# Kernel tuning notes

Measured on AMD Instinct MI355X. Metric: run time of the kernel, lower is better.

The kernel has to match this reference:

```python
import jax, jax.numpy as jnp
import numpy as np

B, H, V, L, NSTYLES = 16, 512, 32000, 3, 5


def setup_inputs() -> dict:
    key = jax.random.key(0)
    ks = jax.random.split(key, 9)
    s = 0.05  # weight init scale
    return {
        "context_vector": jax.random.normal(ks[0], (B, H), dtype=jnp.float32),
        "style_id": jax.random.randint(ks[1], (B,), 0, NSTYLES),
        "style_table": jax.random.normal(ks[2], (NSTYLES, H), dtype=jnp.float32) * s,
        "W_ih": jax.random.normal(ks[3], (L, 4 * H, H), dtype=jnp.float32) * s,
        "W_hh": jax.random.normal(ks[4], (L, 4 * H, H), dtype=jnp.float32) * s,
        "b_ih": jax.random.normal(ks[5], (L, 4 * H), dtype=jnp.float32) * s,
        "b_hh": jax.random.normal(ks[6], (L, 4 * H), dtype=jnp.float32) * s,
        "W_out": jax.random.normal(ks[7], (V, H), dtype=jnp.float32) * s,
        "b_out": jax.random.normal(ks[8], (V,), dtype=jnp.float32) * s,
        "max_length": 100,
    }


def _decode(context_vector, style_id, style_table, W_ih, W_hh, b_ih, b_hh, W_out, b_out, max_length):
    n_layers = W_ih.shape[0]
    x0 = style_table[style_id]                                   # [B, H] style embedding = first input token
    h0 = jnp.broadcast_to(context_vector[None], (n_layers,) + context_vector.shape)  # [L, B, H]
    c0 = jnp.zeros_like(h0)

    def step(carry, _):
        h, c, x = carry
        hs, cs, inp = [], [], x
        for l in range(n_layers):  # small fixed layer loop
            gates = inp @ W_ih[l].T + b_ih[l] + h[l] @ W_hh[l].T + b_hh[l]  # [B, 4H]
            i_g, f_g, g_g, o_g = jnp.split(gates, 4, axis=-1)  # PyTorch i,f,g,o order
            cn = jax.nn.sigmoid(f_g) * c[l] + jax.nn.sigmoid(i_g) * jnp.tanh(g_g)
            hn = jax.nn.sigmoid(o_g) * jnp.tanh(cn)
            hs.append(hn); cs.append(cn); inp = hn
        logits = inp @ W_out.T + b_out                            # [B, V]
        return (jnp.stack(hs), jnp.stack(cs), inp), logits

    _, logits_seq = jax.lax.scan(step, (h0, c0, x0), None, length=max_length)  # [T, B, V]
    # torch stacks [B,1,V] slices along dim=1 -> [B, T, 1, V]
    return jnp.transpose(logits_seq, (1, 0, 2))[:, :, None, :]


def reference(context_vector, style_id, style_table, W_ih, W_hh, b_ih, b_hh, W_out, b_out, max_length):
    return _decode(context_vector, style_id, style_table, W_ih, W_hh, b_ih, b_hh, W_out, b_out, max_length)
```

## Files before the change

### kernel.cpp

```cpp
#include <hip/hip_runtime.h>
#include <hip/hip_bf16.h>
#include <math.h>

#define TSTEPS 100
#define BDIM   16
#define HDIM   512
#define NLAYER 3
#define VDIM   32000
#define NREC   128
#define NGEMM  125
#define NCOLS  256
#define CHUNK  8
#define NCHUNK 13

#define WROW   1032
#define AROW   520

#define POIS8  0xAAAAAAAAAAAAAAAAull

#define SMEM_BYTES 133120

typedef __bf16 bf16x8 __attribute__((ext_vector_type(8)));
typedef float  f32x4  __attribute__((ext_vector_type(4)));
typedef unsigned int u32x4 __attribute__((ext_vector_type(4)));
typedef unsigned long long u64;

__device__ __forceinline__ float sigm_f(float x) { return 1.0f / (1.0f + __expf(-x)); }
__device__ __forceinline__ float tanh_f(float x) { float e = __expf(2.0f * x); return 1.0f - 2.0f / (e + 1.0f); }

template <int N>
__device__ __forceinline__ float spin(float a) {
  #pragma unroll
  for (int i = 0; i < N; ++i) a = __builtin_fmaf(a, 1.0000002f, 1e-30f);
  return a;
}
__device__ __forceinline__ float heat(float a) { return spin<192>(a); }

__device__ __forceinline__ void issue_ld8(u64& dst, const void* p) {
  asm volatile("global_load_dwordx2 %0, %1, off sc0 sc1" : "=&v"(dst) : "v"(p));
}
__device__ __forceinline__ void wait_vm0(void) {
  asm volatile("s_waitcnt vmcnt(0)" ::: "memory");
  __builtin_amdgcn_sched_barrier(0);
}

__device__ __forceinline__ void load_frags_verify(const __bf16* hs, bf16x8* afrag) {
  const char* base = (const char*)hs;
  union U { u32x4 v; u64 u[2]; bf16x8 b; } x[8];
  int guard = 0; float bk = 1.0f;
  while (true) {
    #pragma unroll
    for (int i = 0; i < 8; ++i)
      asm volatile("global_load_dwordx4 %0, %1, off sc0 sc1" : "=&v"(x[i].v) : "v"(base + 64 * i));
    wait_vm0();
    bool ok = true;
    #pragma unroll
    for (int i = 0; i < 8; ++i) ok &= (x[i].u[0] != POIS8) & (x[i].u[1] != POIS8);
    if (__all((int)ok)) break;
    if (++guard > (1 << 17)) break;
    bk = spin<64>(bk);
    asm volatile("" :: "v"(bk));
  }
  #pragma unroll
  for (int i = 0; i < 8; ++i) afrag[i] = x[i].b;
}

__device__ __forceinline__ void detect_block(const __bf16* blkbase, int w64, int lane) {
  const void* sp = (const void*)(blkbase + ((size_t)(lane & 15)) * HDIM + 4 * (w64 + lane));
  int guard = 0; float bk = 1.0f;
  while (true) {
    u64 s;
    issue_ld8(s, sp);
    wait_vm0();
    if (__all((int)(s != POIS8))) break;
    if (++guard > (1 << 17)) break;
    bk = spin<96>(bk);
    asm volatile("" :: "v"(bk));
  }
}

__global__ __launch_bounds__(256) void rgn_kernel(
    const float* __restrict__ ctx,  const int* __restrict__ sid,
    const float* __restrict__ stab,
    const float* __restrict__ wih,  const float* __restrict__ whh,
    const float* __restrict__ bih,  const float* __restrict__ bhh,
    const float* __restrict__ wout, const float* __restrict__ boutg,
    float* __restrict__ out,
    __bf16* h2, __bf16* hbufT, __bf16* wbf)
{
  extern __shared__ char smem[];
  const int tid  = threadIdx.x;
  const int lane = tid & 63;
  const int wid  = tid >> 6;
  const int blk  = blockIdx.x;

  if (blk < NREC) {
    __bf16* Wlds  = (__bf16*)smem;
    float*  biasL = (float*)(smem + 99072);
    float*  pC    = (float*)(smem + 99264);
    const int r = blk;

    for (int idx = tid; idx < NLAYER * 16 * 256; idx += 256) {
      int k4 = idx & 255;
      int rr = (idx >> 8) & 15;
      int l  = idx >> 12;
      int q = rr >> 2, u = rr & 3;
      int grow = q * 512 + 4 * r + u;
      int k = k4 * 4;
      const float* src = (k < 512) ? &wih[((size_t)l * 2048 + grow) * 512 + k]
                                   : &whh[((size_t)l * 2048 + grow) * 512 + (k - 512)];
      float4 v = *(const float4*)src;
      __bf16* d = &Wlds[(l * 16 + rr) * WROW + k];
      d[0] = (__bf16)v.x; d[1] = (__bf16)v.y; d[2] = (__bf16)v.z; d[3] = (__bf16)v.w;
    }
    if (tid < NLAYER * 16) {
      int l = tid >> 4, rr = tid & 15;
      int q = rr >> 2, u = rr & 3;
      int grow = q * 512 + 4 * r + u;
      biasL[tid] = bih[l * 2048 + grow] + bhh[l * 2048 + grow];
    }
    __syncthreads();

    const int m16 = lane & 15;
    const int ko8 = (lane >> 4) * 8;
    float cs = 0.0f;

    int t = 0, l = 0;
    for (int hop = 0; hop < NLAYER * TSTEPS; ++hop) {
      const __bf16* wrow = &Wlds[(l * 16 + m16) * WROW + wid * 256 + ko8];
      bf16x8 bw[8];
      #pragma unroll
      for (int i = 0; i < 8; ++i) bw[i] = *(const bf16x8*)(wrow + 32 * i);

      bf16x8 afrag[8];
      if (wid < 2) {
        const int kp = wid * 256 + ko8;
        if (l == 0) {
          if (t == 0) {
            const int s = sid[m16];
            const float* xs = &stab[s * HDIM + kp];
            #pragma unroll
            for (int i = 0; i < 8; ++i) {
              const float* p = xs + 32 * i; bf16x8 a;
              #pragma unroll
              for (int j = 0; j < 8; ++j) a[j] = (__bf16)p[j];
              afrag[i] = a;
            }
          } else {
            const __bf16* blkbase = &h2[(size_t)(t - 1) * 16 * HDIM];
            detect_block(blkbase, wid * 64, lane);
            load_frags_verify(blkbase + (size_t)m16 * HDIM + kp, afrag);
          }
        } else {
          const __bf16* blkbase = &hbufT[((size_t)t * 2 + (l - 1)) * 16 * HDIM];
          detect_block(blkbase, wid * 64, lane);
          load_frags_verify(blkbase + (size_t)m16 * HDIM + kp, afrag);
        }
      } else {
        const int kp = (wid - 2) * 256 + ko8;
        if (t == 0) {
          const float* hs = &ctx[m16 * HDIM + kp];
          #pragma unroll
          for (int i = 0; i < 8; ++i) {
            const float* p = hs + 32 * i; bf16x8 a;
            #pragma unroll
            for (int j = 0; j < 8; ++j) a[j] = (__bf16)p[j];
            afrag[i] = a;
          }
        } else if (l < 2) {
          load_frags_verify(&hbufT[(((size_t)(t - 1) * 2 + l) * 16 + m16) * HDIM + kp], afrag);
        } else {
          load_frags_verify(&h2[((size_t)(t - 1) * 16 + m16) * HDIM + kp], afrag);
        }
      }

      f32x4 acc = {0.f, 0.f, 0.f, 0.f};
      #pragma unroll
      for (int i = 0; i < 8; ++i)
        acc = __builtin_amdgcn_mfma_f32_16x16x32_bf16(afrag[i], bw[i], acc, 0, 0, 0);

      float* pCp = pC + (hop & 1) * (4 * 16 * 17);
      #pragma unroll
      for (int rr2 = 0; rr2 < 4; ++rr2)
        pCp[(wid * 16 + ((lane >> 4) * 4 + rr2)) * 17 + m16] = acc[rr2];
      __syncthreads();

      if (wid == l) {
        const int m = lane >> 2, u = lane & 3;
        float g[4];
        #pragma unroll
        for (int q = 0; q < 4; ++q) {
          float s = 0.f;
          #pragma unroll
          for (int w = 0; w < 4; ++w) s += pCp[(w * 16 + m) * 17 + q * 4 + u];
          g[q] = s + biasL[l * 16 + q * 4 + u];
        }
        float ig = sigm_f(g[0]), fg = sigm_f(g[1]), gg = tanh_f(g[2]), og = sigm_f(g[3]);
        float cn = fg * cs + ig * gg;
        float hn = og * tanh_f(cn);
        cs = cn;
        union { __bf16 b; unsigned short s; } cv; cv.b = (__bf16)hn;
        unsigned int p2 = (unsigned int)cv.s |
                          ((unsigned int)(unsigned short)__shfl_xor((int)cv.s, 1) << 16);
        unsigned long long p4 = (unsigned long long)p2 |
                          ((unsigned long long)(unsigned int)__shfl_xor((int)p2, 2) << 32);
        if (u == 0) {
          unsigned long long* dst = (l < 2)
            ? (unsigned long long*)&hbufT[(((size_t)t * 2 + l) * 16 + m) * HDIM + 4 * r]
            : (unsigned long long*)&h2[((size_t)t * 16 + m) * HDIM + 4 * r];
          __hip_atomic_store(dst, p4, __ATOMIC_RELAXED, __HIP_MEMORY_SCOPE_AGENT);
        }
      }
      if (++l == NLAYER) { l = 0; ++t; }
    }
  } else if (blk < NREC + NGEMM) {
    __bf16* At = (__bf16*)smem;
    const int g = blk - NREC;
    const int vbase = g * NCOLS;
    const int n16 = lane & 15;
    const int ko8 = (lane >> 4) * 8;
    float hs_acc = 1.0f;

    __bf16* wsl = wbf ? (wbf + (size_t)g * NCOLS * HDIM) : nullptr;
    if (wsl) {
      const float* wsrc = wout + (size_t)vbase * HDIM;
      for (int idx = tid; idx < NCOLS * HDIM / 4; idx += 256) {
        float4 v = *(const float4*)(wsrc + idx * 4);
        union { unsigned long long u; __bf16 b[4]; } rr;
        rr.b[0] = (__bf16)v.x; rr.b[1] = (__bf16)v.y; rr.b[2] = (__bf16)v.z; rr.b[3] = (__bf16)v.w;
        *(unsigned long long*)(wsl + idx * 4) = rr.u;
      }
      __syncthreads();
    }

    for (int ci = 0; ci < NCHUNK; ++ci) {
      const int c0 = ci * CHUNK;
      const int ns = (TSTEPS - c0 < CHUNK) ? (TSTEPS - c0) : CHUNK;
      for (int s = 0; s < ns; ++s) {
        const unsigned long long* src = (const unsigned long long*)&h2[(size_t)(c0 + s) * 16 * HDIM];
        unsigned long long v[8]; unsigned done = 0u; int guard = 0;
        while (done != 0xFFu) {
          #pragma unroll
          for (int it = 0; it < 8; ++it) {
            if (!((done >> it) & 1u)) {
              unsigned long long x =
                  __hip_atomic_load(src + tid + 256 * it, __ATOMIC_RELAXED, __HIP_MEMORY_SCOPE_AGENT);
              if (x != POIS8) { v[it] = x; done |= (1u << it); }
            }
          }
          if (done == 0xFFu) break;
          hs_acc = heat(hs_acc);
          if (++guard > (1 << 20)) break;
        }
        #pragma unroll
        for (int it = 0; it < 8; ++it) {
          const int idx = tid + 256 * it;
          const int m = idx >> 7, k4 = idx & 127;
          *(unsigned long long*)&At[(s * 16 + m) * AROW + k4 * 4] = v[it];
        }
      }
      __syncthreads();
      for (int nt = wid; nt < 16; nt += 4) {
        const int vrow = vbase + nt * 16 + n16;
        bf16x8 bfr[16];
        if (wsl) {
          #pragma unroll
          for (int j = 0; j < 16; ++j)
            bfr[j] = *(const bf16x8*)&wsl[(size_t)(nt * 16 + n16) * HDIM + j * 32 + ko8];
        } else {
          #pragma unroll
          for (int j = 0; j < 16; ++j) {
            const float* p = &wout[(size_t)vrow * HDIM + j * 32 + ko8];
            bf16x8 b;
            #pragma unroll
            for (int e = 0; e < 8; ++e) b[e] = (__bf16)p[e];
            bfr[j] = b;
          }
        }
        const float bo = boutg[vrow];
        for (int s = 0; s < ns; ++s) {
          f32x4 acc = {0.f, 0.f, 0.f, 0.f};
          const __bf16* arow = &At[(s * 16 + n16) * AROW + ko8];
          #pragma unroll
          for (int j = 0; j < 16; ++j) {
            bf16x8 a = *(const bf16x8*)(arow + 32 * j);
            acc = __builtin_amdgcn_mfma_f32_16x16x32_bf16(a, bfr[j], acc, 0, 0, 0);
          }
          const int tt = c0 + s;
          #pragma unroll
          for (int rr2 = 0; rr2 < 4; ++rr2) {
            const int m = (lane >> 4) * 4 + rr2;
            out[((size_t)m * TSTEPS + tt) * VDIM + vrow] = acc[rr2] + bo;
          }
        }
      }
      __syncthreads();
    }
    asm volatile("" :: "v"(hs_acc));
  }
}

extern "C" void kernel_launch(void* const* d_in, const int* in_sizes, int n_in,
                              void* d_out, int out_size, void* d_ws, size_t ws_size,
                              hipStream_t stream) {
  const float* ctx  = (const float*)d_in[0];
  const int*   sid  = (const int*)  d_in[1];
  const float* stab = (const float*)d_in[2];
  const float* wih  = (const float*)d_in[3];
  const float* whh  = (const float*)d_in[4];
  const float* bih  = (const float*)d_in[5];
  const float* bhh  = (const float*)d_in[6];
  const float* wout = (const float*)d_in[7];
  const float* bout = (const float*)d_in[8];
  float* out = (float*)d_out;

  char* ws = (char*)d_ws;
  __bf16* h2    = (__bf16*)ws;
  __bf16* hbufT = (__bf16*)(ws + 1638400);
  size_t  off   = 1638400 + 3276800;
  size_t wb_need = off + (size_t)VDIM * HDIM * 2;
  __bf16* wbf = (ws_size >= wb_need) ? (__bf16*)(ws + off) : nullptr;

  (void)in_sizes; (void)n_in; (void)out_size;
  hipFuncSetAttribute((const void*)rgn_kernel, hipFuncAttributeMaxDynamicSharedMemorySize, SMEM_BYTES);
  rgn_kernel<<<dim3(NREC + NGEMM), dim3(256), SMEM_BYTES, stream>>>(
      ctx, sid, stab, wih, whh, bih, bhh, wout, bout, out, h2, hbufT, wbf);
}
```

Before: 1.491 ms.

## Move recurrent h@W_hh partials off the critical path into helper waves

Restructures the recurrent blocks so wave 0 alone computes the input-side product (full K=512) on the critical path, while waves 1-3 precompute each layer's h_prev@W_hh partial one hop ahead and leave it in LDS. The four-wave cross-wave partial reduction is replaced by a single-wave transpose through LDS before the gate math. This is meant to shorten the serial dependency chain across the 300 layer-steps. The GEMM consumer's per-element atomic polling is replaced by batched loads followed by a wave-wide check. The trade-off is less parallelism inside each hop and heavier per-wave register use.

```diff
diff --git a/kernel.cpp b/kernel.cpp
--- a/kernel.cpp
+++ b/kernel.cpp
@@ -12,12 +12,16 @@
 #define NCOLS  256
 #define CHUNK  8
 #define NCHUNK 13
+#define NHOP   (NLAYER * TSTEPS)
 
 #define WROW   1032
 #define AROW   520
 
 #define POIS8  0xAAAAAAAAAAAAAAAAull
 
+#define OFF_BIAS   99072
+#define OFF_HPART  99264
+#define OFF_TRANS  102336
 #define SMEM_BYTES 133120
 
 typedef __bf16 bf16x8 __attribute__((ext_vector_type(8)));
@@ -44,39 +48,39 @@
   __builtin_amdgcn_sched_barrier(0);
 }
 
-__device__ __forceinline__ void load_frags_verify(const __bf16* hs, bf16x8* afrag) {
+__device__ __forceinline__ void detect128(const __bf16* blkbase, int lane) {
+  const char* sp = (const char*)blkbase + (size_t)(lane & 15) * (HDIM * 2) + 16 * lane;
+  int guard = 0; float bk = 1.0f;
+  while (true) {
+    union { u32x4 v; u64 u[2]; } s;
+    asm volatile("global_load_dwordx4 %0, %1, off sc0 sc1" : "=&v"(s.v) : "v"(sp));
+    wait_vm0();
+    if (__all((int)((s.u[0] != POIS8) & (s.u[1] != POIS8)))) break;
+    if (++guard > (1 << 17)) break;
+    bk = spin<96>(bk);
+    asm volatile("" :: "v"(bk));
+  }
+}
+
+__device__ __forceinline__ void load16_verify(const __bf16* hs, bf16x8* afrag) {
   const char* base = (const char*)hs;
-  union U { u32x4 v; u64 u[2]; bf16x8 b; } x[8];
+  union U { u32x4 v; u64 u[2]; bf16x8 b; } x[16];
   int guard = 0; float bk = 1.0f;
   while (true) {
     #pragma unroll
-    for (int i = 0; i < 8; ++i)
+    for (int i = 0; i < 16; ++i)
       asm volatile("global_load_dwordx4 %0, %1, off sc0 sc1" : "=&v"(x[i].v) : "v"(base + 64 * i));
     wait_vm0();
     bool ok = true;
     #pragma unroll
-    for (int i = 0; i < 8; ++i) ok &= (x[i].u[0] != POIS8) & (x[i].u[1] != POIS8);
+    for (int i = 0; i < 16; ++i) ok &= (x[i].u[0] != POIS8) & (x[i].u[1] != POIS8);
     if (__all((int)ok)) break;
     if (++guard > (1 << 17)) break;
     bk = spin<64>(bk);
     asm volatile("" :: "v"(bk));
   }
   #pragma unroll
-  for (int i = 0; i < 8; ++i) afrag[i] = x[i].b;
-}
-
-__device__ __forceinline__ void detect_block(const __bf16* blkbase, int w64, int lane) {
-  const void* sp = (const void*)(blkbase + ((size_t)(lane & 15)) * HDIM + 4 * (w64 + lane));
-  int guard = 0; float bk = 1.0f;
-  while (true) {
-    u64 s;
-    issue_ld8(s, sp);
-    wait_vm0();
-    if (__all((int)(s != POIS8))) break;
-    if (++guard > (1 << 17)) break;
-    bk = spin<96>(bk);
-    asm volatile("" :: "v"(bk));
-  }
+  for (int i = 0; i < 16; ++i) afrag[i] = x[i].b;
 }
 
 __global__ __launch_bounds__(256) void rgn_kernel(
@@ -96,8 +100,9 @@
 
   if (blk < NREC) {
     __bf16* Wlds  = (__bf16*)smem;
-    float*  biasL = (float*)(smem + 99072);
-    float*  pC    = (float*)(smem + 99264);
+    float*  biasL = (float*)(smem + OFF_BIAS);
+    float*  hpart = (float*)(smem + OFF_HPART);
+    float*  trans = (float*)(smem + OFF_TRANS);
     const int r = blk;
 
     for (int idx = tid; idx < NLAYER * 16 * 256; idx += 256) {
@@ -123,95 +128,103 @@
 
     const int m16 = lane & 15;
     const int ko8 = (lane >> 4) * 8;
-    float cs = 0.0f;
-
-    int t = 0, l = 0;
-    for (int hop = 0; hop < NLAYER * TSTEPS; ++hop) {
-      const __bf16* wrow = &Wlds[(l * 16 + m16) * WROW + wid * 256 + ko8];
-      bf16x8 bw[8];
+
+    if (wid >= 1) {
+      const int l = wid - 1;
+      bf16x8 bw[16], af[16];
       #pragma unroll
-      for (int i = 0; i < 8; ++i) bw[i] = *(const bf16x8*)(wrow + 32 * i);
-
-      bf16x8 afrag[8];
-      if (wid < 2) {
-        const int kp = wid * 256 + ko8;
-        if (l == 0) {
-          if (t == 0) {
-            const int s = sid[m16];
-            const float* xs = &stab[s * HDIM + kp];
+      for (int i = 0; i < 16; ++i)
+        bw[i] = *(const bf16x8*)&Wlds[(l * 16 + m16) * WROW + 512 + i * 32 + ko8];
+      #pragma unroll
+      for (int i = 0; i < 16; ++i) {
+        const float* p = &ctx[m16 * HDIM + i * 32 + ko8];
+        bf16x8 a;
+        #pragma unroll
+        for (int j = 0; j < 8; ++j) a[j] = (__bf16)p[j];
+        af[i] = a;
+      }
+      f32x4 acc = {0.f, 0.f, 0.f, 0.f};
+      #pragma unroll
+      for (int i = 0; i < 16; ++i)
+        acc = __builtin_amdgcn_mfma_f32_16x16x32_bf16(af[i], bw[i], acc, 0, 0, 0);
+      *(f32x4*)&hpart[(l * 64 + lane) * 4] = acc;
+    }
+    float cs0 = 0.f, cs1 = 0.f, cs2 = 0.f;
+    __syncthreads();
+
+    for (int hop = 0; hop < NHOP; ++hop) {
+      const int l = hop % 3, t = hop / 3;
+      if (wid == 0) {
+        bf16x8 bw[16];
+        #pragma unroll
+        for (int i = 0; i < 16; ++i)
+          bw[i] = *(const bf16x8*)&Wlds[(l * 16 + m16) * WROW + i * 32 + ko8];
+        bf16x8 af[16];
+        if (hop == 0) {
+          const int s = sid[m16];
+          #pragma unroll
+          for (int i = 0; i < 16; ++i) {
+            const float* p = &stab[s * HDIM + i * 32 + ko8];
+            bf16x8 a;
             #pragma unroll
-            for (int i = 0; i < 8; ++i) {
-              const float* p = xs + 32 * i; bf16x8 a;
-              #pragma unroll
-              for (int j = 0; j < 8; ++j) a[j] = (__bf16)p[j];
-              afrag[i] = a;
-            }
-          } else {
-            const __bf16* blkbase = &h2[(size_t)(t - 1) * 16 * HDIM];
-            detect_block(blkbase, wid * 64, lane);
-            load_frags_verify(blkbase + (size_t)m16 * HDIM + kp, afrag);
+            for (int j = 0; j < 8; ++j) a[j] = (__bf16)p[j];
+            af[i] = a;
           }
         } else {
-          const __bf16* blkbase = &hbufT[((size_t)t * 2 + (l - 1)) * 16 * HDIM];
-          detect_block(blkbase, wid * 64, lane);
-          load_frags_verify(blkbase + (size_t)m16 * HDIM + kp, afrag);
-        }
-      } else {
-        const int kp = (wid - 2) * 256 + ko8;
-        if (t == 0) {
-          const float* hs = &ctx[m16 * HDIM + kp];
-          #pragma unroll
-          for (int i = 0; i < 8; ++i) {
-            const float* p = hs + 32 * i; bf16x8 a;
-            #pragma unroll
-            for (int j = 0; j < 8; ++j) a[j] = (__bf16)p[j];
-            afrag[i] = a;
-          }
-        } else if (l < 2) {
-          load_frags_verify(&hbufT[(((size_t)(t - 1) * 2 + l) * 16 + m16) * HDIM + kp], afrag);
-        } else {
-          load_frags_verify(&h2[((size_t)(t - 1) * 16 + m16) * HDIM + kp], afrag);
-        }
-      }
-
-      f32x4 acc = {0.f, 0.f, 0.f, 0.f};
-      #pragma unroll
-      for (int i = 0; i < 8; ++i)
-        acc = __builtin_amdgcn_mfma_f32_16x16x32_bf16(afrag[i], bw[i], acc, 0, 0, 0);
-
-      float* pCp = pC + (hop & 1) * (4 * 16 * 17);
-      #pragma unroll
-      for (int rr2 = 0; rr2 < 4; ++rr2)
-        pCp[(wid * 16 + ((lane >> 4) * 4 + rr2)) * 17 + m16] = acc[rr2];
-      __syncthreads();
-
-      if (wid == l) {
+          const __bf16* blkbase = (l == 0)
+            ? &h2[(size_t)(t - 1) * 16 * HDIM]
+            : &hbufT[((size_t)t * 2 + (l - 1)) * 16 * HDIM];
+          detect128(blkbase, lane);
+          load16_verify(blkbase + (size_t)m16 * HDIM + ko8, af);
+        }
+        f32x4 acc = *(const f32x4*)&hpart[(l * 64 + lane) * 4];
+        #pragma unroll
+        for (int i = 0; i < 16; ++i)
+          acc = __builtin_amdgcn_mfma_f32_16x16x32_bf16(af[i], bw[i], acc, 0, 0, 0);
+        const float bia = biasL[l * 16 + m16];
+        #pragma unroll
+        for (int j = 0; j < 4; ++j)
+          trans[((lane >> 4) * 4 + j) * 17 + m16] = acc[j] + bia;
+        asm volatile("s_waitcnt lgkmcnt(0)" ::: "memory");
+        __builtin_amdgcn_sched_barrier(0);
         const int m = lane >> 2, u = lane & 3;
-        float g[4];
-        #pragma unroll
-        for (int q = 0; q < 4; ++q) {
-          float s = 0.f;
-          #pragma unroll
-          for (int w = 0; w < 4; ++w) s += pCp[(w * 16 + m) * 17 + q * 4 + u];
-          g[q] = s + biasL[l * 16 + q * 4 + u];
-        }
-        float ig = sigm_f(g[0]), fg = sigm_f(g[1]), gg = tanh_f(g[2]), og = sigm_f(g[3]);
-        float cn = fg * cs + ig * gg;
+        float g0 = trans[m * 17 + u],     g1 = trans[m * 17 + 4 + u];
+        float g2 = trans[m * 17 + 8 + u], g3 = trans[m * 17 + 12 + u];
+        float ig = sigm_f(g0), fg = sigm_f(g1), gg = tanh_f(g2), og = sigm_f(g3);
+        float cp = (l == 0) ? cs0 : (l == 1) ? cs1 : cs2;
+        float cn = fg * cp + ig * gg;
         float hn = og * tanh_f(cn);
-        cs = cn;
+        if (l == 0) cs0 = cn; else if (l == 1) cs1 = cn; else cs2 = cn;
         union { __bf16 b; unsigned short s; } cv; cv.b = (__bf16)hn;
         unsigned int p2 = (unsigned int)cv.s |
                           ((unsigned int)(unsigned short)__shfl_xor((int)cv.s, 1) << 16);
-        unsigned long long p4 = (unsigned long long)p2 |
-                          ((unsigned long long)(unsigned int)__shfl_xor((int)p2, 2) << 32);
+        u64 p4 = (u64)p2 | ((u64)(unsigned int)__shfl_xor((int)p2, 2) << 32);
         if (u == 0) {
-          unsigned long long* dst = (l < 2)
-            ? (unsigned long long*)&hbufT[(((size_t)t * 2 + l) * 16 + m) * HDIM + 4 * r]
-            : (unsigned long long*)&h2[((size_t)t * 16 + m) * HDIM + 4 * r];
+          u64* dst = (l < 2)
+            ? (u64*)&hbufT[(((size_t)t * 2 + l) * 16 + m) * HDIM + 4 * r]
+            : (u64*)&h2[((size_t)t * 16 + m) * HDIM + 4 * r];
           __hip_atomic_store(dst, p4, __ATOMIC_RELAXED, __HIP_MEMORY_SCOPE_AGENT);
         }
-      }
-      if (++l == NLAYER) { l = 0; ++t; }
+      } else if (hop >= 1 && (hop - 1) % 3 == wid - 1 && hop + 2 < NHOP) {
+        const int ls = wid - 1;
+        const int ts = (hop - 1) / 3;
+        bf16x8 bw[16];
+        #pragma unroll
+        for (int i = 0; i < 16; ++i)
+          bw[i] = *(const bf16x8*)&Wlds[(ls * 16 + m16) * WROW + 512 + i * 32 + ko8];
+        const __bf16* blkbase = (ls < 2)
+          ? &hbufT[((size_t)ts * 2 + ls) * 16 * HDIM]
+          : &h2[(size_t)ts * 16 * HDIM];
+        detect128(blkbase, lane);
+        bf16x8 af[16];
+        load16_verify(blkbase + (size_t)m16 * HDIM + ko8, af);
+        f32x4 acc = {0.f, 0.f, 0.f, 0.f};
+        #pragma unroll
+        for (int i = 0; i < 16; ++i)
+          acc = __builtin_amdgcn_mfma_f32_16x16x32_bf16(af[i], bw[i], acc, 0, 0, 0);
+        *(f32x4*)&hpart[(ls * 64 + lane) * 4] = acc;
+      }
+      __syncthreads();
     }
   } else if (blk < NREC + NGEMM) {
     __bf16* At = (__bf16*)smem;
@@ -237,20 +250,20 @@
       const int c0 = ci * CHUNK;
       const int ns = (TSTEPS - c0 < CHUNK) ? (TSTEPS - c0) : CHUNK;
       for (int s = 0; s < ns; ++s) {
-        const unsigned long long* src = (const unsigned long long*)&h2[(size_t)(c0 + s) * 16 * HDIM];
-        unsigned long long v[8]; unsigned done = 0u; int guard = 0;
-        while (done != 0xFFu) {
-          #pragma unroll
-          for (int it = 0; it < 8; ++it) {
-            if (!((done >> it) & 1u)) {
-              unsigned long long x =
-                  __hip_atomic_load(src + tid + 256 * it, __ATOMIC_RELAXED, __HIP_MEMORY_SCOPE_AGENT);
-              if (x != POIS8) { v[it] = x; done |= (1u << it); }
-            }
-          }
-          if (done == 0xFFu) break;
+        const u64* src = (const u64*)&h2[(size_t)(c0 + s) * 16 * HDIM];
+        u64 v[8];
+        int guard = 0;
+        while (true) {
+          #pragma unroll
+          for (int it = 0; it < 8; ++it)
+            issue_ld8(v[it], (const void*)(src + tid + 256 * it));
+          wait_vm0();
+          bool ok = true;
+          #pragma unroll
+          for (int it = 0; it < 8; ++it) ok &= (v[it] != POIS8);
+          if (__all((int)ok)) break;
           hs_acc = heat(hs_acc);
-          if (++guard > (1 << 20)) break;
+          if (++guard > (1 << 18)) break;
         }
         #pragma unroll
         for (int it = 0; it < 8; ++it) {
```

After: 1.598 ms. +7.2%, slower.
